# Kernel tuning notes

Measured on AMD Instinct MI355X. Metric: run time of the kernel, lower is better.

Reference implementation:

```python
import jax, jax.numpy as jnp
import numpy as np


def _conv(x, w, b, stride):
    # NHWC input, HWIO kernel, SAME padding (matches Keras Conv2D defaults)
    y = jax.lax.conv_general_dilated(
        x, w, window_strides=(stride, stride), padding='SAME',
        dimension_numbers=('NHWC', 'HWIO', 'NHWC'))
    return y + b


def setup_inputs() -> dict:
    key = jax.random.key(0)
    ks = jax.random.split(key, 8)
    D, K = 128, 512  # latent_dim (embedding_dim), num_embeddings
    x = jax.random.uniform(ks[0], (64, 256, 256, 3), dtype=jnp.float32)
    # Encoder params (Conv 4x4 s2 -> 32, Conv 4x4 s2 -> 64, Conv 1x1 -> D)
    w1 = jax.random.normal(ks[1], (4, 4, 3, 32), dtype=jnp.float32) * 0.05
    b1 = jnp.zeros((32,), jnp.float32)
    w2 = jax.random.normal(ks[2], (4, 4, 32, 64), dtype=jnp.float32) * 0.05
    b2 = jnp.zeros((64,), jnp.float32)
    w3 = jax.random.normal(ks[3], (1, 1, 64, D), dtype=jnp.float32) * 0.05
    b3 = jnp.zeros((D,), jnp.float32)
    # VQ codebook: tf.random_uniform_initializer default is U(-0.05, 0.05), shape [D, K]
    embeddings = jax.random.uniform(ks[4], (D, K), minval=-0.05, maxval=0.05,
                                    dtype=jnp.float32)
    return {"x": x, "w1": w1, "b1": b1, "w2": w2, "b2": b2,
            "w3": w3, "b3": b3, "embeddings": embeddings}


def reference(x, w1, b1, w2, b2, w3, b3, embeddings):
    # ---- encoder ----
    h = jax.nn.relu(_conv(x, w1, b1, 2))          # [B, 128, 128, 32]
    h = jax.nn.relu(_conv(h, w2, b2, 2))          # [B,  64,  64, 64]
    z = _conv(h, w3, b3, 1)                       # [B,  64,  64, D]
    # ---- vector quantizer ----
    D = embeddings.shape[0]
    flat = z.reshape(-1, D)                       # [N, D]
    sim = flat @ embeddings                       # [N, K]
    dist = (jnp.sum(flat * flat, axis=1, keepdims=True)
            + jnp.sum(embeddings * embeddings, axis=0)
            - 2.0 * sim)                          # [N, K]
    idx = jnp.argmin(dist, axis=1)                # [N]
    # one_hot(idx) @ embeddings.T  ==  gather rows of embeddings.T
    quantized = jnp.take(embeddings.T, idx, axis=0)  # [N, D]
    return quantized.reshape(z.shape)
```

## Files before the change

kernel.cpp:

```cpp
#include <hip/hip_runtime.h>


__device__ __forceinline__ float fget(const float4& v, int i) {
    return reinterpret_cast<const float*>(&v)[i];
}

__global__ void k_prep(const float* __restrict__ emb,
                       float* __restrict__ eT, float* __restrict__ cvec) {
    int k = blockIdx.x * 256 + threadIdx.x;
    float s = 0.f;
    #pragma unroll 8
    for (int d = 0; d < 128; ++d) {
        float v = emb[d * 512 + k];
        s += v * v;
        eT[k * 128 + d] = v;
    }
    cvec[k] = s;
}

__global__ __launch_bounds__(256) void k_conv1(
        const float* __restrict__ x, const float* __restrict__ w1,
        const float* __restrict__ b1, float* __restrict__ h1, int b0) {
    int t = threadIdx.x;
    int p = blockIdx.x * 256 + t;
    int ow = p & 127, oh = (p >> 7) & 127, b = b0 + (p >> 14);
    float acc[32];
    #pragma unroll
    for (int c = 0; c < 32; ++c) acc[c] = b1[c];
    #pragma unroll
    for (int kh = 0; kh < 4; ++kh) {
        int ih = oh * 2 - 1 + kh;
        if ((unsigned)ih >= 256u) continue;
        #pragma unroll
        for (int kw = 0; kw < 4; ++kw) {
            int iw = ow * 2 - 1 + kw;
            if ((unsigned)iw >= 256u) continue;
            const float* xp = x + (((size_t)(b * 256 + ih) * 256 + iw) * 3);
            float x0 = xp[0], x1 = xp[1], x2 = xp[2];
            const float* wp = w1 + (kh * 4 + kw) * 96;
            #pragma unroll
            for (int c = 0; c < 32; ++c)
                acc[c] += x0 * wp[c] + x1 * wp[32 + c] + x2 * wp[64 + c];
        }
    }
    float4* op = (float4*)(h1 + (size_t)p * 32);
    #pragma unroll
    for (int c4 = 0; c4 < 8; ++c4) {
        float4 v;
        v.x = fmaxf(acc[c4 * 4 + 0], 0.f);
        v.y = fmaxf(acc[c4 * 4 + 1], 0.f);
        v.z = fmaxf(acc[c4 * 4 + 2], 0.f);
        v.w = fmaxf(acc[c4 * 4 + 3], 0.f);
        op[c4] = v;
    }
}

#define XROW 580
__global__ __launch_bounds__(256) void k_conv2(
        const float* __restrict__ h1, const float* __restrict__ w2,
        const float* __restrict__ b2, float* __restrict__ h2) {
    __shared__ float xl[18 * XROW];
    __shared__ float wl[8192];
    __shared__ float bl[64];
    int t = threadIdx.x;
    int blk = blockIdx.x;
    int tx = blk & 7, ty = (blk >> 3) & 7, b = blk >> 6;
    int oh0 = ty * 8, ow0 = tx * 8;
    int ih0 = oh0 * 2 - 1, iw0 = ow0 * 2 - 1;
    if (t < 64) bl[t] = b2[t];
    for (int i = t; i < 2592; i += 256) {
        int f = i & 7;
        int pos = i >> 3;
        int r = pos / 18, c = pos - r * 18;
        int ih = ih0 + r, iw = iw0 + c;
        float4 v = make_float4(0.f, 0.f, 0.f, 0.f);
        if ((unsigned)ih < 128u && (unsigned)iw < 128u)
            v = *(const float4*)(h1 + ((size_t)((b * 128 + ih) * 128 + iw) * 32 + f * 4));
        *(float4*)(xl + r * XROW + c * 32 + f * 4) = v;
    }
    int tc = t & 15, tr = t >> 4;
    int g = ((tr & 3) << 2) | (tr >> 2);
    int olr = g >> 1, olc0 = (g & 1) * 4;
    __syncthreads();
    float4 bv = ((const float4*)bl)[tc];
    float4 acc[4];
    #pragma unroll
    for (int j = 0; j < 4; ++j) acc[j] = bv;
    for (int kh = 0; kh < 4; ++kh) {
        __syncthreads();
        const float4* wsrc = (const float4*)(w2 + kh * 8192);
        for (int i = t; i < 2048; i += 256) ((float4*)wl)[i] = wsrc[i];
        __syncthreads();
        #pragma unroll
        for (int kw = 0; kw < 4; ++kw) {
            #pragma unroll
            for (int ci4 = 0; ci4 < 8; ++ci4) {
                float4 xq[4], wq[4];
                #pragma unroll
                for (int j = 0; j < 4; ++j)
                    xq[j] = *(const float4*)(xl + (olr * 2 + kh) * XROW +
                                             ((olc0 + j) * 2 + kw) * 32 + ci4 * 4);
                #pragma unroll
                for (int i = 0; i < 4; ++i)
                    wq[i] = ((const float4*)wl)[(kw * 32 + ci4 * 4 + i) * 16 + tc];
                #pragma unroll
                for (int i = 0; i < 4; ++i) {
                    #pragma unroll
                    for (int j = 0; j < 4; ++j) {
                        float xv = fget(xq[j], i);
                        acc[j].x += xv * wq[i].x;
                        acc[j].y += xv * wq[i].y;
                        acc[j].z += xv * wq[i].z;
                        acc[j].w += xv * wq[i].w;
                    }
                }
            }
        }
    }
    int oh = oh0 + olr;
    #pragma unroll
    for (int j = 0; j < 4; ++j) {
        int ow = ow0 + olc0 + j;
        float4 v = acc[j];
        v.x = fmaxf(v.x, 0.f); v.y = fmaxf(v.y, 0.f);
        v.z = fmaxf(v.z, 0.f); v.w = fmaxf(v.w, 0.f);
        *(float4*)(h2 + ((size_t)((b * 64 + oh) * 64 + ow) * 64 + tc * 4)) = v;
    }
}

__global__ __launch_bounds__(256) void k_vq(
        const float* __restrict__ h2, const float* __restrict__ w3,
        const float* __restrict__ b3, const float* __restrict__ emb,
        const float* __restrict__ eT, const float* __restrict__ cvec,
        float* __restrict__ out, int px_base) {
    __shared__ float zl[64 * 132];
    __shared__ float buf[8192];
    __shared__ float cl[512];
    __shared__ float b3l[128];
    int t = threadIdx.x;
    size_t px0 = (size_t)blockIdx.x * 64;
    {
        const float4* src = (const float4*)(h2 + px0 * 64);
        for (int i = t; i < 1024; i += 256) ((float4*)buf)[i] = src[i];
    }
    if (t < 32) ((float4*)b3l)[t] = ((const float4*)b3)[t];
    if (t >= 128 && t < 256) ((float4*)cl)[t - 128] = ((const float4*)cvec)[t - 128];
    for (int dh = 0; dh < 2; ++dh) {
        __syncthreads();
        for (int i = t; i < 1024; i += 256) {
            int ci = i >> 4, dq = i & 15;
            ((float4*)buf)[1024 + i] =
                *(const float4*)(w3 + ci * 128 + dh * 64 + dq * 4);
        }
        __syncthreads();
        #pragma unroll
        for (int it = 0; it < 4; ++it) {
            int idx = t + it * 256;
            int px = idx >> 4, dq = idx & 15;
            float4 a = ((const float4*)b3l)[dh * 16 + dq];
            const float* hrow = buf + px * 64;
            const float4* wcol = ((const float4*)buf) + 1024;
            #pragma unroll 8
            for (int ci = 0; ci < 64; ++ci) {
                float hv = hrow[ci];
                float4 wv = wcol[ci * 16 + dq];
                a.x += hv * wv.x; a.y += hv * wv.y;
                a.z += hv * wv.z; a.w += hv * wv.w;
            }
            *(float4*)(zl + px * 132 + dh * 64 + dq * 4) = a;
        }
    }
    int kc = t & 15, pr = t >> 4;
    float minv[4]; int mini[4];
    #pragma unroll
    for (int j = 0; j < 4; ++j) { minv[j] = 3.4e38f; mini[j] = 0; }
    for (int kb = 0; kb < 8; ++kb) {
        __syncthreads();
        for (int i = t; i < 2048; i += 256) {
            int d = i >> 4, kq = i & 15;
            ((float4*)buf)[i] = *(const float4*)(emb + d * 512 + kb * 64 + kq * 4);
        }
        __syncthreads();
        float4 s[4];
        #pragma unroll
        for (int j = 0; j < 4; ++j) s[j] = make_float4(0.f, 0.f, 0.f, 0.f);
        #pragma unroll 4
        for (int d4 = 0; d4 < 32; ++d4) {
            float4 zq[4], eq[4];
            #pragma unroll
            for (int j = 0; j < 4; ++j)
                zq[j] = *(const float4*)(zl + (pr * 4 + j) * 132 + d4 * 4);
            #pragma unroll
            for (int i = 0; i < 4; ++i)
                eq[i] = ((const float4*)buf)[(d4 * 4 + i) * 16 + kc];
            #pragma unroll
            for (int i = 0; i < 4; ++i) {
                #pragma unroll
                for (int j = 0; j < 4; ++j) {
                    float zv = fget(zq[j], i);
                    s[j].x += zv * eq[i].x;
                    s[j].y += zv * eq[i].y;
                    s[j].z += zv * eq[i].z;
                    s[j].w += zv * eq[i].w;
                }
            }
        }
        int k0 = kb * 64 + kc * 4;
        #pragma unroll
        for (int j = 0; j < 4; ++j) {
            float d0 = cl[k0 + 0] - 2.f * s[j].x;
            float d1 = cl[k0 + 1] - 2.f * s[j].y;
            float d2 = cl[k0 + 2] - 2.f * s[j].z;
            float d3 = cl[k0 + 3] - 2.f * s[j].w;
            if (d0 < minv[j]) { minv[j] = d0; mini[j] = k0 + 0; }
            if (d1 < minv[j]) { minv[j] = d1; mini[j] = k0 + 1; }
            if (d2 < minv[j]) { minv[j] = d2; mini[j] = k0 + 2; }
            if (d3 < minv[j]) { minv[j] = d3; mini[j] = k0 + 3; }
        }
    }
    #pragma unroll
    for (int j = 0; j < 4; ++j) {
        float v = minv[j]; int ki = mini[j];
        #pragma unroll
        for (int off = 8; off > 0; off >>= 1) {
            float ov = __shfl_xor(v, off, 16);
            int oi = __shfl_xor(ki, off, 16);
            if (ov < v || (ov == v && oi < ki)) { v = ov; ki = oi; }
        }
        const float4* src = (const float4*)(eT + (size_t)ki * 128);
        float4* dst = (float4*)(out + ((size_t)px_base + px0 + pr * 4 + j) * 128);
        dst[kc] = src[kc];
        dst[kc + 16] = src[kc + 16];
    }
}

extern "C" void kernel_launch(void* const* d_in, const int* in_sizes, int n_in,
                              void* d_out, int out_size, void* d_ws, size_t ws_size,
                              hipStream_t stream) {
    const float* x   = (const float*)d_in[0];
    const float* w1  = (const float*)d_in[1];
    const float* b1  = (const float*)d_in[2];
    const float* w2  = (const float*)d_in[3];
    const float* b2  = (const float*)d_in[4];
    const float* w3  = (const float*)d_in[5];
    const float* b3  = (const float*)d_in[6];
    const float* emb = (const float*)d_in[7];
    float* out = (float*)d_out;

    const size_t H1_FULL = 33554432;
    const size_t H2_FULL = 16777216;
    const size_t FIXEDF  = 65536 + 512;

    int nchunk = 1;
    while (nchunk < 64 &&
           (FIXEDF + (H1_FULL + H2_FULL) / (size_t)nchunk) * 4 > ws_size)
        nchunk <<= 1;
    int bpc = 64 / nchunk;

    float* ws = (float*)d_ws;
    float* eT = ws;
    float* cv = eT + 65536;
    float* h1 = cv + 512;
    float* h2 = h1 + H1_FULL / (size_t)nchunk;

    k_prep<<<2, 256, 0, stream>>>(emb, eT, cv);
    int nblk = 4096 / nchunk;
    for (int ch = 0; ch < nchunk; ++ch) {
        int b0 = ch * bpc;
        k_conv1<<<nblk, 256, 0, stream>>>(x, w1, b1, h1, b0);
        k_conv2<<<nblk, 256, 0, stream>>>(h1, w2, b2, h2);
        k_vq   <<<nblk, 256, 0, stream>>>(h2, w3, b3, emb, eT, cv, out,
                                          b0 * 4096);
    }
}
```

Before: 1.149 ms.

## Rewrite VQ kernel as one-pixel-per-thread with register-resident latent vector

```diff
diff --git a/kernel.cpp b/kernel.cpp
--- a/kernel.cpp
+++ b/kernel.cpp
@@ -128,110 +128,58 @@
     }
 }
 
-__global__ __launch_bounds__(256) void k_vq(
+__global__ __launch_bounds__(256, 3) void k_vq(
         const float* __restrict__ h2, const float* __restrict__ w3,
-        const float* __restrict__ b3, const float* __restrict__ emb,
-        const float* __restrict__ eT, const float* __restrict__ cvec,
-        float* __restrict__ out, int px_base) {
-    __shared__ float zl[64 * 132];
-    __shared__ float buf[8192];
-    __shared__ float cl[512];
-    __shared__ float b3l[128];
-    int t = threadIdx.x;
-    size_t px0 = (size_t)blockIdx.x * 64;
-    {
-        const float4* src = (const float4*)(h2 + px0 * 64);
-        for (int i = t; i < 1024; i += 256) ((float4*)buf)[i] = src[i];
-    }
-    if (t < 32) ((float4*)b3l)[t] = ((const float4*)b3)[t];
-    if (t >= 128 && t < 256) ((float4*)cl)[t - 128] = ((const float4*)cvec)[t - 128];
-    for (int dh = 0; dh < 2; ++dh) {
-        __syncthreads();
-        for (int i = t; i < 1024; i += 256) {
-            int ci = i >> 4, dq = i & 15;
-            ((float4*)buf)[1024 + i] =
-                *(const float4*)(w3 + ci * 128 + dh * 64 + dq * 4);
-        }
-        __syncthreads();
-        #pragma unroll
-        for (int it = 0; it < 4; ++it) {
-            int idx = t + it * 256;
-            int px = idx >> 4, dq = idx & 15;
-            float4 a = ((const float4*)b3l)[dh * 16 + dq];
-            const float* hrow = buf + px * 64;
-            const float4* wcol = ((const float4*)buf) + 1024;
-            #pragma unroll 8
-            for (int ci = 0; ci < 64; ++ci) {
-                float hv = hrow[ci];
-                float4 wv = wcol[ci * 16 + dq];
-                a.x += hv * wv.x; a.y += hv * wv.y;
-                a.z += hv * wv.z; a.w += hv * wv.w;
-            }
-            *(float4*)(zl + px * 132 + dh * 64 + dq * 4) = a;
-        }
-    }
-    int kc = t & 15, pr = t >> 4;
-    float minv[4]; int mini[4];
-    #pragma unroll
-    for (int j = 0; j < 4; ++j) { minv[j] = 3.4e38f; mini[j] = 0; }
-    for (int kb = 0; kb < 8; ++kb) {
-        __syncthreads();
-        for (int i = t; i < 2048; i += 256) {
-            int d = i >> 4, kq = i & 15;
-            ((float4*)buf)[i] = *(const float4*)(emb + d * 512 + kb * 64 + kq * 4);
-        }
-        __syncthreads();
-        float4 s[4];
-        #pragma unroll
-        for (int j = 0; j < 4; ++j) s[j] = make_float4(0.f, 0.f, 0.f, 0.f);
-        #pragma unroll 4
-        for (int d4 = 0; d4 < 32; ++d4) {
-            float4 zq[4], eq[4];
+        const float* __restrict__ b3, const float* __restrict__ eT,
+        const float* __restrict__ cvec, float* __restrict__ out,
+        long long px_base) {
+    int p = blockIdx.x * 256 + threadIdx.x;
+    const float* h2row = h2 + (size_t)p * 64;
+
+    float z[128];
+    #pragma unroll
+    for (int d = 0; d < 128; ++d) z[d] = b3[d];
+    for (int ci = 0; ci < 64; ci += 4) {
+        float4 hv = *(const float4*)(h2row + ci);
+        const float* w0 = w3 + ci * 128;
+        #pragma unroll
+        for (int j = 0; j < 4; ++j) {
+            float h = fget(hv, j);
+            const float* wr = w0 + j * 128;
             #pragma unroll
-            for (int j = 0; j < 4; ++j)
-                zq[j] = *(const float4*)(zl + (pr * 4 + j) * 132 + d4 * 4);
-            #pragma unroll
-            for (int i = 0; i < 4; ++i)
-                eq[i] = ((const float4*)buf)[(d4 * 4 + i) * 16 + kc];
-            #pragma unroll
-            for (int i = 0; i < 4; ++i) {
-                #pragma unroll
-                for (int j = 0; j < 4; ++j) {
-                    float zv = fget(zq[j], i);
-                    s[j].x += zv * eq[i].x;
-                    s[j].y += zv * eq[i].y;
-                    s[j].z += zv * eq[i].z;
-                    s[j].w += zv * eq[i].w;
-                }
-            }
-        }
-        int k0 = kb * 64 + kc * 4;
-        #pragma unroll
-        for (int j = 0; j < 4; ++j) {
-            float d0 = cl[k0 + 0] - 2.f * s[j].x;
-            float d1 = cl[k0 + 1] - 2.f * s[j].y;
-            float d2 = cl[k0 + 2] - 2.f * s[j].z;
-            float d3 = cl[k0 + 3] - 2.f * s[j].w;
-            if (d0 < minv[j]) { minv[j] = d0; mini[j] = k0 + 0; }
-            if (d1 < minv[j]) { minv[j] = d1; mini[j] = k0 + 1; }
-            if (d2 < minv[j]) { minv[j] = d2; mini[j] = k0 + 2; }
-            if (d3 < minv[j]) { minv[j] = d3; mini[j] = k0 + 3; }
-        }
-    }
-    #pragma unroll
-    for (int j = 0; j < 4; ++j) {
-        float v = minv[j]; int ki = mini[j];
-        #pragma unroll
-        for (int off = 8; off > 0; off >>= 1) {
-            float ov = __shfl_xor(v, off, 16);
-            int oi = __shfl_xor(ki, off, 16);
-            if (ov < v || (ov == v && oi < ki)) { v = ov; ki = oi; }
-        }
-        const float4* src = (const float4*)(eT + (size_t)ki * 128);
-        float4* dst = (float4*)(out + ((size_t)px_base + px0 + pr * 4 + j) * 128);
-        dst[kc] = src[kc];
-        dst[kc + 16] = src[kc + 16];
-    }
+            for (int d = 0; d < 128; ++d) z[d] += h * wr[d];
+        }
+    }
+
+    float minv = 3.4e38f;
+    int mini = 0;
+    for (int k = 0; k < 512; k += 4) {
+        const float* e0 = eT + (size_t)k * 128;
+        const float* e1 = e0 + 128;
+        const float* e2 = e0 + 256;
+        const float* e3 = e0 + 384;
+        float s0 = 0.f, s1 = 0.f, s2 = 0.f, s3 = 0.f;
+        #pragma unroll
+        for (int d = 0; d < 128; ++d) {
+            s0 += z[d] * e0[d];
+            s1 += z[d] * e1[d];
+            s2 += z[d] * e2[d];
+            s3 += z[d] * e3[d];
+        }
+        float d0 = cvec[k + 0] - 2.f * s0;
+        float d1 = cvec[k + 1] - 2.f * s1;
+        float d2 = cvec[k + 2] - 2.f * s2;
+        float d3 = cvec[k + 3] - 2.f * s3;
+        if (d0 < minv) { minv = d0; mini = k + 0; }
+        if (d1 < minv) { minv = d1; mini = k + 1; }
+        if (d2 < minv) { minv = d2; mini = k + 2; }
+        if (d3 < minv) { minv = d3; mini = k + 3; }
+    }
+
+    const float4* src = (const float4*)(eT + (size_t)mini * 128);
+    float4* dst = (float4*)(out + ((size_t)(px_base + p)) * 128);
+    #pragma unroll
+    for (int q = 0; q < 32; ++q) dst[q] = src[q];
 }
 
 extern "C" void kernel_launch(void* const* d_in, const int* in_sizes, int n_in,
@@ -265,11 +213,12 @@
 
     k_prep<<<2, 256, 0, stream>>>(emb, eT, cv);
     int nblk = 4096 / nchunk;
+    int nblk_vq = 1024 / nchunk;
     for (int ch = 0; ch < nchunk; ++ch) {
         int b0 = ch * bpc;
         k_conv1<<<nblk, 256, 0, stream>>>(x, w1, b1, h1, b0);
         k_conv2<<<nblk, 256, 0, stream>>>(h1, w2, b2, h2);
-        k_vq   <<<nblk, 256, 0, stream>>>(h2, w3, b3, emb, eT, cv, out,
-                                          b0 * 4096);
-    }
-}
+        k_vq   <<<nblk_vq, 256, 0, stream>>>(h2, w3, b3, eT, cv, out,
+                                             (long long)b0 * 4096);
+    }
+}
```

New measurement: 1.686 ms. +46.7%, slower.
